# Performance work log

Hardware: AMD Instinct MI355X
Metric: run time of the kernel (lower is better)

Reference implementation:

```python
import jax, jax.numpy as jnp
import numpy as np

B, V, E, H, K = 4, 8192, 256, 8, 6  # batch, n_points, embed_dim, heads, knn


def setup_inputs() -> dict:
    key = jax.random.key(0)
    k1, k2, k3, k4 = jax.random.split(key, 4)
    scale = 1.0 / np.sqrt(E)
    return {
        "x": jax.random.normal(k1, (B, V, E), jnp.float32),
        "x_v": jax.random.normal(k2, (B, V, 3), jnp.float32),
        "in_proj_w": jax.random.normal(k3, (3 * E, E), jnp.float32) * scale,
        "out_proj_w": jax.random.normal(k4, (E, E), jnp.float32) * scale,
    }


def reference(x, x_v, in_proj_w, out_proj_w):
    Bn, Vn, En = x.shape
    Dh = En // H

    # ---- knn_points(x_v, x_v, K, return_sorted=True): squared L2 dists ----
    sq = jnp.sum(x_v * x_v, axis=-1)  # [B,V]
    d = sq[:, :, None] + sq[:, None, :] - 2.0 * jnp.einsum('bvc,bwc->bvw', x_v, x_v)
    _, idx = jax.lax.top_k(-d, K)  # [B,V,K], ascending distance (self first)

    # ---- knn_gather(x, idx) ----
    k = jax.vmap(lambda xb, ib: xb[ib])(x, idx)  # [B,V,K,E]
    v = k - x[:, :, None, :]                      # use_direction=True

    # ---- tiny MHA per point (Q len 1, KV len K), bias=False, eval (no dropout) ----
    Wq, Wk, Wv = jnp.split(in_proj_w, 3, axis=0)  # each [E,E]
    qp = (x @ Wq.T).reshape(Bn, Vn, H, Dh)
    kp = jnp.einsum('bvke,fe->bvkf', k, Wk).reshape(Bn, Vn, K, H, Dh)
    vp = jnp.einsum('bvke,fe->bvkf', v, Wv).reshape(Bn, Vn, K, H, Dh)
    scores = jnp.einsum('bvhd,bvkhd->bvhk', qp, kp) / np.sqrt(Dh)
    attn = jax.nn.softmax(scores, axis=-1)  # [B,V,H,K]
    out = jnp.einsum('bvhk,bvkhd->bvhd', attn, vp).reshape(Bn, Vn, En)
    out = out @ out_proj_w.T
    x_out = x + out

    # ---- scatter_reduce mean of head-averaged attention weights ----
    x_w = attn.mean(axis=2)  # [B,V,K] (MHA averages weights over heads)
    idx_f = idx.reshape(Bn, Vn * K)
    src = x_w.reshape(Bn, Vn * K)
    sums = jax.vmap(lambda i, s: jax.ops.segment_sum(s, i, num_segments=Vn))(idx_f, src)
    ones = jnp.ones((Vn * K,), jnp.float32)
    counts = jax.vmap(lambda i: jax.ops.segment_sum(ones, i, num_segments=Vn))(idx_f)
    # torch scatter_reduce_ 'mean' with include_self=True on a zeros tensor:
    # mean includes the initial 0, so denominator is count + 1.
    xw_out = (sums / (counts + 1.0))[..., None]  # [B,V,1]

    return x_out, xw_out
```

## Files before the change

kernel.cpp:

```cpp
#include <hip/hip_runtime.h>
#include <hip/hip_bf16.h>
#include <math.h>

#define BB 4
#define VV 8192
#define EE 256
#define HH 8
#define KK 6
#define NP (BB*VV)

#define OFF_XV4 0
#define OFF_KNN 524288
#define OFF_XWS 1310720
#define OFF_XWC 1441792
#define OFF_XB  1572864
#define OFF_WB  18350080
#define OFF_QKV 18874368
#define OFF_AO  69206016

typedef float f32x4 __attribute__((ext_vector_type(4)));
typedef __bf16 bf16x8 __attribute__((ext_vector_type(8)));

__device__ __forceinline__ unsigned short f2b(float f) {
  __hip_bfloat16 h = __float2bfloat16(f);
  return *reinterpret_cast<unsigned short*>(&h);
}
__device__ __forceinline__ float b2f(unsigned short u) {
  unsigned v = ((unsigned)u) << 16;
  return __uint_as_float(v);
}

__global__ void prep_kernel(const float* __restrict__ xv, float4* __restrict__ xv4,
                            float* __restrict__ xw_sum, float* __restrict__ xw_cnt) {
  int i = blockIdx.x * blockDim.x + threadIdx.x;
  if (i >= NP) return;
  float x0 = xv[i*3+0], x1 = xv[i*3+1], x2 = xv[i*3+2];
  float sq = __fadd_rn(__fadd_rn(__fmul_rn(x0,x0), __fmul_rn(x1,x1)), __fmul_rn(x2,x2));
  xv4[i] = make_float4(x0, x1, x2, sq);
  xw_sum[i] = 0.f;
  xw_cnt[i] = 0.f;
}

__global__ void cvt_bf16(const float* __restrict__ src, unsigned short* __restrict__ dst, int n4) {
  int i = blockIdx.x * blockDim.x + threadIdx.x;
  if (i >= n4) return;
  float4 v = ((const float4*)src)[i];
  ushort4 o;
  o.x = f2b(v.x); o.y = f2b(v.y); o.z = f2b(v.z); o.w = f2b(v.w);
  ((ushort4*)dst)[i] = o;
}


__device__ __forceinline__ unsigned long long pack_key(float dist, int j) {
  unsigned du = __float_as_uint(dist);
  du ^= (unsigned)((int)du >> 31) | 0x80000000u;
  return ((unsigned long long)du << 32) | (unsigned)j;
}

#define INSU(key) \
  if (key < k5) { \
    bool b4 = key < k4, b3 = key < k3, b2 = key < k2, b1 = key < k1, b0 = key < k0; \
    k5 = b4 ? k4 : key; \
    k4 = b4 ? (b3 ? k3 : key) : k4; \
    k3 = b3 ? (b2 ? k2 : key) : k3; \
    k2 = b2 ? (b1 ? k1 : key) : k2; \
    k1 = b1 ? (b0 ? k0 : key) : k1; \
    k0 = b0 ? key : k0; \
  }

__global__ __launch_bounds__(256) void knn_kernel(const float4* __restrict__ xv4,
                                                  int* __restrict__ knn_idx) {
  __shared__ float4 tile[1024];
  int tid = threadIdx.x;
  int qb = tid & 31;
  int c = tid >> 5;
  int q = blockIdx.x * 32 + qb;
  int base = (q >> 13) << 13;

  float4 me = xv4[q];
  float mx = me.x, my = me.y, mz = me.z, sqq = me.w;

  float d0=INFINITY,d1=INFINITY,d2=INFINITY,d3=INFINITY,d4=INFINITY,d5=INFINITY;
  int   i0=0x7fffffff,i1=0x7fffffff,i2=0x7fffffff,i3=0x7fffffff,i4=0x7fffffff,i5=0x7fffffff;

  for (int t = 0; t < 8; ++t) {
    __syncthreads();
#pragma unroll
    for (int u = 0; u < 4; ++u)
      tile[tid + u*256] = xv4[base + t*1024 + tid + u*256];
    __syncthreads();

    const float4* cp = &tile[c * 128];
    int jbase = t*1024 + c*128;
#pragma unroll 8
    for (int it = 0; it < 128; ++it) {
      float4 p = cp[it];
      float dot  = __fadd_rn(__fadd_rn(__fmul_rn(mx,p.x), __fmul_rn(my,p.y)), __fmul_rn(mz,p.z));
      float dist = __fsub_rn(__fadd_rn(sqq, p.w), __fmul_rn(2.0f, dot));
      if (dist < d5) {
        int j = jbase + it;
        bool b4 = dist < d4, b3 = dist < d3, b2 = dist < d2, b1 = dist < d1, b0 = dist < d0;
        d5 = b4 ? d4 : dist;            i5 = b4 ? i4 : j;
        d4 = b4 ? (b3 ? d3 : dist) : d4; i4 = b4 ? (b3 ? i3 : j) : i4;
        d3 = b3 ? (b2 ? d2 : dist) : d3; i3 = b3 ? (b2 ? i2 : j) : i3;
        d2 = b2 ? (b1 ? d1 : dist) : d2; i2 = b2 ? (b1 ? i1 : j) : i2;
        d1 = b1 ? (b0 ? d0 : dist) : d1; i1 = b1 ? (b0 ? i0 : j) : i1;
        d0 = b0 ? dist : d0;            i0 = b0 ? j : i0;
      }
    }
  }

  __syncthreads();
  unsigned long long* mk = reinterpret_cast<unsigned long long*>(tile);
  if (c > 0) {
    int o = qb*43 + (c-1)*6;
    mk[o+0]=pack_key(d0,i0); mk[o+1]=pack_key(d1,i1); mk[o+2]=pack_key(d2,i2);
    mk[o+3]=pack_key(d3,i3); mk[o+4]=pack_key(d4,i4); mk[o+5]=pack_key(d5,i5);
  }
  __syncthreads();
  if (c == 0) {
    unsigned long long k0=pack_key(d0,i0),k1=pack_key(d1,i1),k2=pack_key(d2,i2),
                       k3=pack_key(d3,i3),k4=pack_key(d4,i4),k5=pack_key(d5,i5);
    for (int s = 0; s < 42; ++s) {
      unsigned long long key = mk[qb*43 + s];
      INSU(key);
    }
    knn_idx[q*6+0] = (int)(unsigned)k0;
    knn_idx[q*6+1] = (int)(unsigned)k1;
    knn_idx[q*6+2] = (int)(unsigned)k2;
    knn_idx[q*6+3] = (int)(unsigned)k3;
    knn_idx[q*6+4] = (int)(unsigned)k4;
    knn_idx[q*6+5] = (int)(unsigned)k5;
  }
}

template<bool OUT_BF16>
__global__ __launch_bounds__(256) void gemm_bf16(const unsigned short* __restrict__ A,
                                                 const unsigned short* __restrict__ Bw,
                                                 void* __restrict__ Cv,
                                                 const float* __restrict__ R,
                                                 int ldc) {
  __shared__ unsigned short ABs[8192];
  int tid = threadIdx.x;
  int lane = tid & 63;
  int w = tid >> 6;
  int bm = blockIdx.x * 128;
  int bn = blockIdx.y * 128;
  int wr = w >> 1, wc = w & 1;

  f32x4 acc[4][4] = {};

  for (int ks = 0; ks < 8; ++ks) {
    int k0 = ks * 32;
    __syncthreads();
#pragma unroll
    for (int t = 0; t < 4; ++t) {
      int bg = (t*4 + w) * 64;
      int g = bg + lane;
      const unsigned short* src;
      if (bg < 512) {
        int r = g >> 2, kb = g & 3;
        src = A + (size_t)(bm + r) * 256 + k0 + kb*8;
      } else {
        int g2 = g - 512;
        int r = g2 >> 2, kb = g2 & 3;
        src = Bw + (size_t)(bn + r) * 256 + k0 + kb*8;
      }
      __builtin_amdgcn_global_load_lds(
        (const __attribute__((address_space(1))) unsigned int*)src,
        (__attribute__((address_space(3))) unsigned int*)&ABs[bg*8],
        16, 0, 0);
    }
    __syncthreads();

    bf16x8 af[4], bfr[4];
#pragma unroll
    for (int m = 0; m < 4; ++m)
      af[m] = *(const bf16x8*)&ABs[(wr*64 + m*16 + (lane&15))*32 + (lane>>4)*8];
#pragma unroll
    for (int n = 0; n < 4; ++n)
      bfr[n] = *(const bf16x8*)&ABs[4096 + (wc*64 + n*16 + (lane&15))*32 + (lane>>4)*8];
#pragma unroll
    for (int m = 0; m < 4; ++m)
#pragma unroll
      for (int n = 0; n < 4; ++n)
        acc[m][n] = __builtin_amdgcn_mfma_f32_16x16x32_bf16(af[m], bfr[n], acc[m][n], 0, 0, 0);
  }

  int rb = bm + wr*64 + (lane>>4)*4;
  int cb = bn + wc*64 + (lane&15);
#pragma unroll
  for (int m = 0; m < 4; ++m)
#pragma unroll
    for (int n = 0; n < 4; ++n)
#pragma unroll
      for (int i = 0; i < 4; ++i) {
        int row = rb + m*16 + i;
        int col = cb + n*16;
        float v = acc[m][n][i];
        if (OUT_BF16) {
          ((unsigned short*)Cv)[(size_t)row*ldc + col] = f2b(v);
        } else {
          ((float*)Cv)[(size_t)row*ldc + col] = v + R[(size_t)row*ldc + col];
        }
      }
}

__global__ __launch_bounds__(256) void attn_kernel(const unsigned short* __restrict__ QKV,
                                                   const int* __restrict__ knn_idx,
                                                   unsigned short* __restrict__ attn_out,
                                                   float* __restrict__ xw_sum,
                                                   float* __restrict__ xw_cnt) {
  int p = blockIdx.x * 4 + (threadIdx.x >> 6);
  int lane = threadIdx.x & 63;
  size_t gbase = (size_t)(p >> 13) << 13;
  size_t prow = (size_t)p * 768;

  ushort4 qv = *(const ushort4*)&QKV[prow + lane*4];
  ushort4 sv = *(const ushort4*)&QKV[prow + 512 + lane*4];
  float qx=b2f(qv.x), qy=b2f(qv.y), qz=b2f(qv.z), qw=b2f(qv.w);
  float sx=b2f(sv.x), sy=b2f(sv.y), sz=b2f(sv.z), sw=b2f(sv.w);

  int idx[KK];
#pragma unroll
  for (int j = 0; j < KK; ++j) idx[j] = knn_idx[p*KK + j];

  float s[KK];
  float vx[KK], vy[KK], vz[KK], vw[KK];
#pragma unroll
  for (int j = 0; j < KK; ++j) {
    size_t r = (gbase + idx[j]) * 768;
    ushort4 kv = *(const ushort4*)&QKV[r + 256 + lane*4];
    ushort4 vv = *(const ushort4*)&QKV[r + 512 + lane*4];
    float t = qx*b2f(kv.x) + qy*b2f(kv.y) + qz*b2f(kv.z) + qw*b2f(kv.w);
    t += __shfl_xor(t, 1);
    t += __shfl_xor(t, 2);
    t += __shfl_xor(t, 4);
    s[j] = t * 0.17677669529663687f;
    vx[j] = b2f(vv.x); vy[j] = b2f(vv.y); vz[j] = b2f(vv.z); vw[j] = b2f(vv.w);
  }

  float m = s[0];
#pragma unroll
  for (int j = 1; j < KK; ++j) m = fmaxf(m, s[j]);
  float e[KK], denom = 0.f;
#pragma unroll
  for (int j = 0; j < KK; ++j) { e[j] = expf(s[j] - m); denom += e[j]; }
  float inv = 1.0f / denom;
#pragma unroll
  for (int j = 0; j < KK; ++j) e[j] *= inv;

  float ox=0.f, oy=0.f, oz=0.f, ow=0.f;
#pragma unroll
  for (int j = 0; j < KK; ++j) {
    float a = e[j];
    ox += a * (vx[j] - sx);
    oy += a * (vy[j] - sy);
    oz += a * (vz[j] - sz);
    ow += a * (vw[j] - sw);
  }
  ushort4 ov;
  ov.x = f2b(ox); ov.y = f2b(oy); ov.z = f2b(oz); ov.w = f2b(ow);
  *(ushort4*)&attn_out[(size_t)p * 256 + lane*4] = ov;

#pragma unroll
  for (int j = 0; j < KK; ++j) {
    float t = e[j];
    t += __shfl_xor(t, 8);
    t += __shfl_xor(t, 16);
    t += __shfl_xor(t, 32);
    if (lane == 0) {
      atomicAdd(&xw_sum[gbase + idx[j]], t * 0.125f);
      atomicAdd(&xw_cnt[gbase + idx[j]], 1.0f);
    }
  }
}

__global__ void finalize_xw(const float* __restrict__ xw_sum,
                            const float* __restrict__ xw_cnt,
                            float* __restrict__ out) {
  int i = blockIdx.x * blockDim.x + threadIdx.x;
  if (i < NP) out[i] = xw_sum[i] / (xw_cnt[i] + 1.0f);
}

extern "C" void kernel_launch(void* const* d_in, const int* in_sizes, int n_in,
                              void* d_out, int out_size, void* d_ws, size_t ws_size,
                              hipStream_t stream) {
  const float* x     = (const float*)d_in[0];
  const float* xv    = (const float*)d_in[1];
  const float* w_in  = (const float*)d_in[2];
  const float* w_out = (const float*)d_in[3];
  float* out = (float*)d_out;

  char* ws = (char*)d_ws;
  float4*         xv4    = (float4*)(ws + OFF_XV4);
  int*            knn    = (int*)(ws + OFF_KNN);
  float*          xw_sum = (float*)(ws + OFF_XWS);
  float*          xw_cnt = (float*)(ws + OFF_XWC);
  unsigned short* xb     = (unsigned short*)(ws + OFF_XB);
  unsigned short* wb     = (unsigned short*)(ws + OFF_WB);
  unsigned short* qkv    = (unsigned short*)(ws + OFF_QKV);
  unsigned short* ao     = (unsigned short*)(ws + OFF_AO);

  prep_kernel<<<(NP + 255) / 256, 256, 0, stream>>>(xv, xv4, xw_sum, xw_cnt);
  cvt_bf16<<<(NP*256/4 + 255)/256, 256, 0, stream>>>(x, xb, NP*256/4);
  cvt_bf16<<<(768*256/4 + 255)/256, 256, 0, stream>>>(w_in, wb, 768*256/4);
  cvt_bf16<<<(256*256/4 + 255)/256, 256, 0, stream>>>(w_out, wb + 768*256, 256*256/4);

  knn_kernel<<<NP / 32, 256, 0, stream>>>(xv4, knn);

  gemm_bf16<true><<<dim3(NP/128, 768/128), 256, 0, stream>>>(xb, wb, qkv, nullptr, 768);

  attn_kernel<<<NP / 4, 256, 0, stream>>>(qkv, knn, ao, xw_sum, xw_cnt);

  gemm_bf16<false><<<dim3(NP/128, 256/128), 256, 0, stream>>>(ao, wb + 768*256, out, x, 256);

  finalize_xw<<<NP / 256, 256, 0, stream>>>(xw_sum, xw_cnt, out + (size_t)NP * EE);
}
```

Measured before the change: 281.4 us.

## Restructure kNN to one query per thread with two candidate chunks and merge kernel

The kNN search changes from 8 threads per query, each scanning a slice with an in-block shared-memory merge, to one query per thread. Each block loads a 4096-point chunk into shared memory once, and a grid dimension of 2 covers the two halves of each batch. Each thread writes 6 partial top-k keys per chunk to a global workspace, and a separate merge kernel combines the 12 candidates. This removes the repeated tile reloads, barriers and serial 42-step merge, but adds a kernel launch and a global round-trip for the partial results. Grid parallelism also drops from 1024 blocks to 256, and the 64 KB shared tile limits occupancy.

```diff
diff --git a/kernel.cpp b/kernel.cpp
--- a/kernel.cpp
+++ b/kernel.cpp
@@ -9,14 +9,15 @@
 #define KK 6
 #define NP (BB*VV)
 
-#define OFF_XV4 0
-#define OFF_KNN 524288
-#define OFF_XWS 1310720
-#define OFF_XWC 1441792
-#define OFF_XB  1572864
-#define OFF_WB  18350080
-#define OFF_QKV 18874368
-#define OFF_AO  69206016
+#define OFF_XV4  0
+#define OFF_KNN  524288
+#define OFF_XWS  1310720
+#define OFF_XWC  1441792
+#define OFF_XB   1572864
+#define OFF_WB   18350080
+#define OFF_QKV  18874368
+#define OFF_AO   69206016
+#define OFF_PART 85983232
 
 typedef float f32x4 __attribute__((ext_vector_type(4)));
 typedef __bf16 bf16x8 __attribute__((ext_vector_type(8)));
@@ -69,69 +70,65 @@
   }
 
 __global__ __launch_bounds__(256) void knn_kernel(const float4* __restrict__ xv4,
-                                                  int* __restrict__ knn_idx) {
-  __shared__ float4 tile[1024];
+                                                  unsigned long long* __restrict__ part) {
+  __shared__ float4 tile[4096];
   int tid = threadIdx.x;
-  int qb = tid & 31;
-  int c = tid >> 5;
-  int q = blockIdx.x * 32 + qb;
+  int q = blockIdx.x * 256 + tid;
   int base = (q >> 13) << 13;
+  int chunk = blockIdx.y;
+  int cbase = base + chunk * 4096;
 
   float4 me = xv4[q];
   float mx = me.x, my = me.y, mz = me.z, sqq = me.w;
 
+#pragma unroll
+  for (int u = 0; u < 16; ++u)
+    tile[tid + u*256] = xv4[cbase + tid + u*256];
+  __syncthreads();
+
   float d0=INFINITY,d1=INFINITY,d2=INFINITY,d3=INFINITY,d4=INFINITY,d5=INFINITY;
   int   i0=0x7fffffff,i1=0x7fffffff,i2=0x7fffffff,i3=0x7fffffff,i4=0x7fffffff,i5=0x7fffffff;
 
-  for (int t = 0; t < 8; ++t) {
-    __syncthreads();
-#pragma unroll
-    for (int u = 0; u < 4; ++u)
-      tile[tid + u*256] = xv4[base + t*1024 + tid + u*256];
-    __syncthreads();
-
-    const float4* cp = &tile[c * 128];
-    int jbase = t*1024 + c*128;
+  int jbase = chunk * 4096;
 #pragma unroll 8
-    for (int it = 0; it < 128; ++it) {
-      float4 p = cp[it];
-      float dot  = __fadd_rn(__fadd_rn(__fmul_rn(mx,p.x), __fmul_rn(my,p.y)), __fmul_rn(mz,p.z));
-      float dist = __fsub_rn(__fadd_rn(sqq, p.w), __fmul_rn(2.0f, dot));
-      if (dist < d5) {
-        int j = jbase + it;
-        bool b4 = dist < d4, b3 = dist < d3, b2 = dist < d2, b1 = dist < d1, b0 = dist < d0;
-        d5 = b4 ? d4 : dist;            i5 = b4 ? i4 : j;
-        d4 = b4 ? (b3 ? d3 : dist) : d4; i4 = b4 ? (b3 ? i3 : j) : i4;
-        d3 = b3 ? (b2 ? d2 : dist) : d3; i3 = b3 ? (b2 ? i2 : j) : i3;
-        d2 = b2 ? (b1 ? d1 : dist) : d2; i2 = b2 ? (b1 ? i1 : j) : i2;
-        d1 = b1 ? (b0 ? d0 : dist) : d1; i1 = b1 ? (b0 ? i0 : j) : i1;
-        d0 = b0 ? dist : d0;            i0 = b0 ? j : i0;
-      }
+  for (int it = 0; it < 4096; ++it) {
+    float4 p = tile[it];
+    float dot  = __fadd_rn(__fadd_rn(__fmul_rn(mx,p.x), __fmul_rn(my,p.y)), __fmul_rn(mz,p.z));
+    float dist = __fsub_rn(__fadd_rn(sqq, p.w), __fmul_rn(2.0f, dot));
+    if (dist < d5) {
+      int j = jbase + it;
+      bool b4 = dist < d4, b3 = dist < d3, b2 = dist < d2, b1 = dist < d1, b0 = dist < d0;
+      d5 = b4 ? d4 : dist;             i5 = b4 ? i4 : j;
+      d4 = b4 ? (b3 ? d3 : dist) : d4; i4 = b4 ? (b3 ? i3 : j) : i4;
+      d3 = b3 ? (b2 ? d2 : dist) : d3; i3 = b3 ? (b2 ? i2 : j) : i3;
+      d2 = b2 ? (b1 ? d1 : dist) : d2; i2 = b2 ? (b1 ? i1 : j) : i2;
+      d1 = b1 ? (b0 ? d0 : dist) : d1; i1 = b1 ? (b0 ? i0 : j) : i1;
+      d0 = b0 ? dist : d0;             i0 = b0 ? j : i0;
     }
   }
 
-  __syncthreads();
-  unsigned long long* mk = reinterpret_cast<unsigned long long*>(tile);
-  if (c > 0) {
-    int o = qb*43 + (c-1)*6;
-    mk[o+0]=pack_key(d0,i0); mk[o+1]=pack_key(d1,i1); mk[o+2]=pack_key(d2,i2);
-    mk[o+3]=pack_key(d3,i3); mk[o+4]=pack_key(d4,i4); mk[o+5]=pack_key(d5,i5);
-  }
-  __syncthreads();
-  if (c == 0) {
-    unsigned long long k0=pack_key(d0,i0),k1=pack_key(d1,i1),k2=pack_key(d2,i2),
-                       k3=pack_key(d3,i3),k4=pack_key(d4,i4),k5=pack_key(d5,i5);
-    for (int s = 0; s < 42; ++s) {
-      unsigned long long key = mk[qb*43 + s];
-      INSU(key);
-    }
-    knn_idx[q*6+0] = (int)(unsigned)k0;
-    knn_idx[q*6+1] = (int)(unsigned)k1;
-    knn_idx[q*6+2] = (int)(unsigned)k2;
-    knn_idx[q*6+3] = (int)(unsigned)k3;
-    knn_idx[q*6+4] = (int)(unsigned)k4;
-    knn_idx[q*6+5] = (int)(unsigned)k5;
-  }
+  unsigned long long* o = part + (size_t)q * 12 + chunk * 6;
+  o[0] = pack_key(d0, i0); o[1] = pack_key(d1, i1); o[2] = pack_key(d2, i2);
+  o[3] = pack_key(d3, i3); o[4] = pack_key(d4, i4); o[5] = pack_key(d5, i5);
+}
+
+__global__ void knn_merge(const unsigned long long* __restrict__ part,
+                          int* __restrict__ knn_idx) {
+  int q = blockIdx.x * 256 + threadIdx.x;
+  if (q >= NP) return;
+  unsigned long long k0=~0ull,k1=~0ull,k2=~0ull,k3=~0ull,k4=~0ull,k5=~0ull;
+  const unsigned long long* pp = part + (size_t)q * 12;
+#pragma unroll
+  for (int s = 0; s < 12; ++s) {
+    unsigned long long key = pp[s];
+    INSU(key);
+  }
+  knn_idx[q*6+0] = (int)(unsigned)k0;
+  knn_idx[q*6+1] = (int)(unsigned)k1;
+  knn_idx[q*6+2] = (int)(unsigned)k2;
+  knn_idx[q*6+3] = (int)(unsigned)k3;
+  knn_idx[q*6+4] = (int)(unsigned)k4;
+  knn_idx[q*6+5] = (int)(unsigned)k5;
 }
 
 template<bool OUT_BF16>
@@ -293,21 +290,23 @@
   float* out = (float*)d_out;
 
   char* ws = (char*)d_ws;
-  float4*         xv4    = (float4*)(ws + OFF_XV4);
-  int*            knn    = (int*)(ws + OFF_KNN);
-  float*          xw_sum = (float*)(ws + OFF_XWS);
-  float*          xw_cnt = (float*)(ws + OFF_XWC);
-  unsigned short* xb     = (unsigned short*)(ws + OFF_XB);
-  unsigned short* wb     = (unsigned short*)(ws + OFF_WB);
-  unsigned short* qkv    = (unsigned short*)(ws + OFF_QKV);
-  unsigned short* ao     = (unsigned short*)(ws + OFF_AO);
+  float4*             xv4    = (float4*)(ws + OFF_XV4);
+  int*                knn    = (int*)(ws + OFF_KNN);
+  float*              xw_sum = (float*)(ws + OFF_XWS);
+  float*              xw_cnt = (float*)(ws + OFF_XWC);
+  unsigned short*     xb     = (unsigned short*)(ws + OFF_XB);
+  unsigned short*     wb     = (unsigned short*)(ws + OFF_WB);
+  unsigned short*     qkv    = (unsigned short*)(ws + OFF_QKV);
+  unsigned short*     ao     = (unsigned short*)(ws + OFF_AO);
+  unsigned long long* part   = (unsigned long long*)(ws + OFF_PART);
 
   prep_kernel<<<(NP + 255) / 256, 256, 0, stream>>>(xv, xv4, xw_sum, xw_cnt);
   cvt_bf16<<<(NP*256/4 + 255)/256, 256, 0, stream>>>(x, xb, NP*256/4);
   cvt_bf16<<<(768*256/4 + 255)/256, 256, 0, stream>>>(w_in, wb, 768*256/4);
   cvt_bf16<<<(256*256/4 + 255)/256, 256, 0, stream>>>(w_out, wb + 768*256, 256*256/4);
 
-  knn_kernel<<<NP / 32, 256, 0, stream>>>(xv4, knn);
+  knn_kernel<<<dim3(NP/256, 2), 256, 0, stream>>>(xv4, part);
+  knn_merge<<<NP/256, 256, 0, stream>>>(part, knn);
 
   gemm_bf16<true><<<dim3(NP/128, 768/128), 256, 0, stream>>>(xb, wb, qkv, nullptr, 768);
 
```

New measurement: 478.5 us. 70.1% more time.

## Replace brute-force KNN with x-sorted sweep and early-exit pruning

Applied to the files above, without the earlier changes.

Bitonic-sorts points by x-coordinate per batch in shared memory, then each query scans outward in sorted order from its position with four interleaved directional threads. A thread stops once the x-gap squared exceeds its current sixth-best distance plus a margin. The four partial top-6 lists are merged in shared memory and written back through the sort permutation. This replaces the O(V^2) all-pairs distance scan with a pruned sweep, adding a single-block-per-batch sort and divergent, data-dependent loop lengths.

```diff
diff --git a/kernel.cpp b/kernel.cpp
--- a/kernel.cpp
+++ b/kernel.cpp
@@ -9,14 +9,16 @@
 #define KK 6
 #define NP (BB*VV)
 
-#define OFF_XV4 0
-#define OFF_KNN 524288
-#define OFF_XWS 1310720
-#define OFF_XWC 1441792
-#define OFF_XB  1572864
-#define OFF_WB  18350080
-#define OFF_QKV 18874368
-#define OFF_AO  69206016
+#define OFF_XV4  0
+#define OFF_KNN  524288
+#define OFF_XWS  1310720
+#define OFF_XWC  1441792
+#define OFF_XB   1572864
+#define OFF_WB   18350080
+#define OFF_QKV  18874368
+#define OFF_AO   69206016
+#define OFF_SXV  85983232
+#define OFF_SPM  86507520
 
 typedef float f32x4 __attribute__((ext_vector_type(4)));
 typedef __bf16 bf16x8 __attribute__((ext_vector_type(8)));
@@ -28,6 +30,19 @@
 __device__ __forceinline__ float b2f(unsigned short u) {
   unsigned v = ((unsigned)u) << 16;
   return __uint_as_float(v);
+}
+
+__device__ __forceinline__ unsigned sortable(float f) {
+  unsigned u = __float_as_uint(f);
+  return u ^ ((unsigned)((int)u >> 31) | 0x80000000u);
+}
+__device__ __forceinline__ unsigned long long pack_key(float dist, int j) {
+  return ((unsigned long long)sortable(dist) << 32) | (unsigned)j;
+}
+__device__ __forceinline__ float unpack_dist(unsigned long long k) {
+  unsigned du = (unsigned)(k >> 32);
+  du = (du & 0x80000000u) ? (du ^ 0x80000000u) : ~du;
+  return __uint_as_float(du);
 }
 
 __global__ void prep_kernel(const float* __restrict__ xv, float4* __restrict__ xv4,
@@ -50,12 +65,42 @@
   ((ushort4*)dst)[i] = o;
 }
 
-
-__device__ __forceinline__ unsigned long long pack_key(float dist, int j) {
-  unsigned du = __float_as_uint(dist);
-  du ^= (unsigned)((int)du >> 31) | 0x80000000u;
-  return ((unsigned long long)du << 32) | (unsigned)j;
-}
+__global__ __launch_bounds__(1024) void sort_kernel(const float4* __restrict__ xv4,
+                                                    float4* __restrict__ sxv4,
+                                                    int* __restrict__ sperm) {
+  __shared__ unsigned long long keys[VV];
+  int tid = threadIdx.x;
+  int bb = blockIdx.x * VV;
+#pragma unroll
+  for (int t = 0; t < 8; ++t) {
+    int i = tid + t*1024;
+    keys[i] = ((unsigned long long)sortable(xv4[bb + i].x) << 32) | (unsigned)i;
+  }
+  for (int k = 2; k <= VV; k <<= 1) {
+    for (int jj = k >> 1; jj > 0; jj >>= 1) {
+      __syncthreads();
+#pragma unroll
+      for (int t = 0; t < 4; ++t) {
+        int c = tid + t*1024;
+        int i = ((c & ~(jj-1)) << 1) | (c & (jj-1));
+        int p = i + jj;
+        bool up = ((i & k) == 0);
+        unsigned long long a = keys[i], b = keys[p];
+        if ((a > b) == up) { keys[i] = b; keys[p] = a; }
+      }
+    }
+  }
+  __syncthreads();
+#pragma unroll
+  for (int t = 0; t < 8; ++t) {
+    int r = tid + t*1024;
+    int idx = (int)(unsigned)keys[r];
+    sxv4[bb + r] = xv4[bb + idx];
+    sperm[bb + r] = idx;
+  }
+}
+
+#define MARGIN 1e-3f
 
 #define INSU(key) \
   if (key < k5) { \
@@ -68,69 +113,60 @@
     k0 = b0 ? key : k0; \
   }
 
-__global__ __launch_bounds__(256) void knn_kernel(const float4* __restrict__ xv4,
-                                                  int* __restrict__ knn_idx) {
-  __shared__ float4 tile[1024];
-  int tid = threadIdx.x;
-  int qb = tid & 31;
-  int c = tid >> 5;
-  int q = blockIdx.x * 32 + qb;
-  int base = (q >> 13) << 13;
-
-  float4 me = xv4[q];
+__global__ __launch_bounds__(256) void knn_scan(const float4* __restrict__ sxv4,
+                                                const int* __restrict__ sperm,
+                                                int* __restrict__ knn_idx) {
+  __shared__ unsigned long long sk[64][25];
+  int lane = threadIdx.x & 63;
+  int side = threadIdx.x >> 6;
+  int g = blockIdx.x * 64 + lane;
+  int bb = (g >> 13) << 13;
+
+  float4 me = sxv4[g];
   float mx = me.x, my = me.y, mz = me.z, sqq = me.w;
-
-  float d0=INFINITY,d1=INFINITY,d2=INFINITY,d3=INFINITY,d4=INFINITY,d5=INFINITY;
-  int   i0=0x7fffffff,i1=0x7fffffff,i2=0x7fffffff,i3=0x7fffffff,i4=0x7fffffff,i5=0x7fffffff;
-
-  for (int t = 0; t < 8; ++t) {
-    __syncthreads();
-#pragma unroll
-    for (int u = 0; u < 4; ++u)
-      tile[tid + u*256] = xv4[base + t*1024 + tid + u*256];
-    __syncthreads();
-
-    const float4* cp = &tile[c * 128];
-    int jbase = t*1024 + c*128;
-#pragma unroll 8
-    for (int it = 0; it < 128; ++it) {
-      float4 p = cp[it];
-      float dot  = __fadd_rn(__fadd_rn(__fmul_rn(mx,p.x), __fmul_rn(my,p.y)), __fmul_rn(mz,p.z));
-      float dist = __fsub_rn(__fadd_rn(sqq, p.w), __fmul_rn(2.0f, dot));
-      if (dist < d5) {
-        int j = jbase + it;
-        bool b4 = dist < d4, b3 = dist < d3, b2 = dist < d2, b1 = dist < d1, b0 = dist < d0;
-        d5 = b4 ? d4 : dist;            i5 = b4 ? i4 : j;
-        d4 = b4 ? (b3 ? d3 : dist) : d4; i4 = b4 ? (b3 ? i3 : j) : i4;
-        d3 = b3 ? (b2 ? d2 : dist) : d3; i3 = b3 ? (b2 ? i2 : j) : i3;
-        d2 = b2 ? (b1 ? d1 : dist) : d2; i2 = b2 ? (b1 ? i1 : j) : i2;
-        d1 = b1 ? (b0 ? d0 : dist) : d1; i1 = b1 ? (b0 ? i0 : j) : i1;
-        d0 = b0 ? dist : d0;            i0 = b0 ? j : i0;
-      }
-    }
-  }
-
+  int myidx = sperm[g];
+
+  unsigned long long k0=~0ull,k1=~0ull,k2=~0ull,k3=~0ull,k4=~0ull,k5=~0ull;
+  float d5f = __uint_as_float(0x7f7fffffu);
+
+  int step = (side & 2) ? 2 : -2;
+  int p0 = (side == 0) ? g - 1 : (side == 1) ? g - 2 : (side == 2) ? g : g + 1;
+
+  for (int p = p0; (unsigned)(p - bb) < (unsigned)VV; p += step) {
+    float4 c = sxv4[p];
+    float dx = mx - c.x;
+    if (dx * dx > d5f + MARGIN) break;
+    float dot  = __fadd_rn(__fadd_rn(__fmul_rn(mx,c.x), __fmul_rn(my,c.y)), __fmul_rn(mz,c.z));
+    float dist = __fsub_rn(__fadd_rn(sqq, c.w), __fmul_rn(2.0f, dot));
+    unsigned long long key = pack_key(dist, sperm[p]);
+    if (key < k5) {
+      bool b4 = key < k4, b3 = key < k3, b2 = key < k2, b1 = key < k1, b0 = key < k0;
+      k5 = b4 ? k4 : key;
+      k4 = b4 ? (b3 ? k3 : key) : k4;
+      k3 = b3 ? (b2 ? k2 : key) : k3;
+      k2 = b2 ? (b1 ? k1 : key) : k2;
+      k1 = b1 ? (b0 ? k0 : key) : k1;
+      k0 = b0 ? key : k0;
+      if (k5 != ~0ull) d5f = unpack_dist(k5);
+    }
+  }
+
+  sk[lane][side*6+0]=k0; sk[lane][side*6+1]=k1; sk[lane][side*6+2]=k2;
+  sk[lane][side*6+3]=k3; sk[lane][side*6+4]=k4; sk[lane][side*6+5]=k5;
   __syncthreads();
-  unsigned long long* mk = reinterpret_cast<unsigned long long*>(tile);
-  if (c > 0) {
-    int o = qb*43 + (c-1)*6;
-    mk[o+0]=pack_key(d0,i0); mk[o+1]=pack_key(d1,i1); mk[o+2]=pack_key(d2,i2);
-    mk[o+3]=pack_key(d3,i3); mk[o+4]=pack_key(d4,i4); mk[o+5]=pack_key(d5,i5);
-  }
-  __syncthreads();
-  if (c == 0) {
-    unsigned long long k0=pack_key(d0,i0),k1=pack_key(d1,i1),k2=pack_key(d2,i2),
-                       k3=pack_key(d3,i3),k4=pack_key(d4,i4),k5=pack_key(d5,i5);
-    for (int s = 0; s < 42; ++s) {
-      unsigned long long key = mk[qb*43 + s];
+  if (side == 0) {
+#pragma unroll
+    for (int s = 6; s < 24; ++s) {
+      unsigned long long key = sk[lane][s];
       INSU(key);
     }
-    knn_idx[q*6+0] = (int)(unsigned)k0;
-    knn_idx[q*6+1] = (int)(unsigned)k1;
-    knn_idx[q*6+2] = (int)(unsigned)k2;
-    knn_idx[q*6+3] = (int)(unsigned)k3;
-    knn_idx[q*6+4] = (int)(unsigned)k4;
-    knn_idx[q*6+5] = (int)(unsigned)k5;
+    int grow = bb + myidx;
+    knn_idx[grow*6+0] = (int)(unsigned)k0;
+    knn_idx[grow*6+1] = (int)(unsigned)k1;
+    knn_idx[grow*6+2] = (int)(unsigned)k2;
+    knn_idx[grow*6+3] = (int)(unsigned)k3;
+    knn_idx[grow*6+4] = (int)(unsigned)k4;
+    knn_idx[grow*6+5] = (int)(unsigned)k5;
   }
 }
 
@@ -301,13 +337,16 @@
   unsigned short* wb     = (unsigned short*)(ws + OFF_WB);
   unsigned short* qkv    = (unsigned short*)(ws + OFF_QKV);
   unsigned short* ao     = (unsigned short*)(ws + OFF_AO);
+  float4*         sxv4   = (float4*)(ws + OFF_SXV);
+  int*            sperm  = (int*)(ws + OFF_SPM);
 
   prep_kernel<<<(NP + 255) / 256, 256, 0, stream>>>(xv, xv4, xw_sum, xw_cnt);
   cvt_bf16<<<(NP*256/4 + 255)/256, 256, 0, stream>>>(x, xb, NP*256/4);
   cvt_bf16<<<(768*256/4 + 255)/256, 256, 0, stream>>>(w_in, wb, 768*256/4);
   cvt_bf16<<<(256*256/4 + 255)/256, 256, 0, stream>>>(w_out, wb + 768*256, 256*256/4);
 
-  knn_kernel<<<NP / 32, 256, 0, stream>>>(xv4, knn);
+  sort_kernel<<<BB, 1024, 0, stream>>>(xv4, sxv4, sperm);
+  knn_scan<<<NP/64, 256, 0, stream>>>(sxv4, sperm, knn);
 
   gemm_bf16<true><<<dim3(NP/128, 768/128), 256, 0, stream>>>(xb, wb, qkv, nullptr, 768);
 
```

New measurement: 881.9 us. +213.5%, slower.

## Fuse KNN and QKV GEMM into one interleaved launch with paired-point packed math

Applied to the files above, without the earlier changes.

Merges the KNN search and the QKV projection GEMM into a single front kernel. Blocks are interleaved 2:3 between KNN work and GEMM tiles so the ALU-bound KNN and the MFMA-bound GEMM can run concurrently on the device. The point coordinates are re-laid out in pairs (x0,x1,y0,y1,z0,z1,sq0,sq1) so the distance computation can use two-wide packed float math with contraction disabled. This adds register and LDS pressure from the shared kernel and branch divergence between block roles.

```diff
diff --git a/kernel.cpp b/kernel.cpp
--- a/kernel.cpp
+++ b/kernel.cpp
@@ -19,6 +19,7 @@
 #define OFF_AO  69206016
 
 typedef float f32x4 __attribute__((ext_vector_type(4)));
+typedef float f32x2 __attribute__((ext_vector_type(2)));
 typedef __bf16 bf16x8 __attribute__((ext_vector_type(8)));
 
 __device__ __forceinline__ unsigned short f2b(float f) {
@@ -30,31 +31,22 @@
   return __uint_as_float(v);
 }
 
-__global__ void prep_kernel(const float* __restrict__ xv, float4* __restrict__ xv4,
-                            float* __restrict__ xw_sum, float* __restrict__ xw_cnt) {
-  int i = blockIdx.x * blockDim.x + threadIdx.x;
-  if (i >= NP) return;
-  float x0 = xv[i*3+0], x1 = xv[i*3+1], x2 = xv[i*3+2];
-  float sq = __fadd_rn(__fadd_rn(__fmul_rn(x0,x0), __fmul_rn(x1,x1)), __fmul_rn(x2,x2));
-  xv4[i] = make_float4(x0, x1, x2, sq);
-  xw_sum[i] = 0.f;
-  xw_cnt[i] = 0.f;
-}
-
-__global__ void cvt_bf16(const float* __restrict__ src, unsigned short* __restrict__ dst, int n4) {
-  int i = blockIdx.x * blockDim.x + threadIdx.x;
-  if (i >= n4) return;
-  float4 v = ((const float4*)src)[i];
-  ushort4 o;
-  o.x = f2b(v.x); o.y = f2b(v.y); o.z = f2b(v.z); o.w = f2b(v.w);
-  ((ushort4*)dst)[i] = o;
-}
-
-
+__device__ __forceinline__ unsigned sortable(float f) {
+  unsigned u = __float_as_uint(f);
+  return u ^ ((unsigned)((int)u >> 31) | 0x80000000u);
+}
 __device__ __forceinline__ unsigned long long pack_key(float dist, int j) {
-  unsigned du = __float_as_uint(dist);
-  du ^= (unsigned)((int)du >> 31) | 0x80000000u;
-  return ((unsigned long long)du << 32) | (unsigned)j;
+  return ((unsigned long long)sortable(dist) << 32) | (unsigned)j;
+}
+
+#define INSERT6(dist,j) { \
+  bool b4 = dist < d4, b3 = dist < d3, b2 = dist < d2, b1 = dist < d1, b0 = dist < d0; \
+  d5 = b4 ? d4 : dist;             i5 = b4 ? i4 : j; \
+  d4 = b4 ? (b3 ? d3 : dist) : d4; i4 = b4 ? (b3 ? i3 : j) : i4; \
+  d3 = b3 ? (b2 ? d2 : dist) : d3; i3 = b3 ? (b2 ? i2 : j) : i3; \
+  d2 = b2 ? (b1 ? d1 : dist) : d2; i2 = b2 ? (b1 ? i1 : j) : i2; \
+  d1 = b1 ? (b0 ? d0 : dist) : d1; i1 = b1 ? (b0 ? i0 : j) : i1; \
+  d0 = b0 ? dist : d0;             i0 = b0 ? j : i0; \
 }
 
 #define INSU(key) \
@@ -68,78 +60,175 @@
     k0 = b0 ? key : k0; \
   }
 
-__global__ __launch_bounds__(256) void knn_kernel(const float4* __restrict__ xv4,
-                                                  int* __restrict__ knn_idx) {
-  __shared__ float4 tile[1024];
+__global__ void prep_kernel(const float* __restrict__ xv, float* __restrict__ xv4p,
+                            float* __restrict__ xw_sum, float* __restrict__ xw_cnt) {
+  int i = blockIdx.x * blockDim.x + threadIdx.x;
+  if (i >= NP) return;
+  float x0 = xv[i*3+0], x1 = xv[i*3+1], x2 = xv[i*3+2];
+  float sq = __fadd_rn(__fadd_rn(__fmul_rn(x0,x0), __fmul_rn(x1,x1)), __fmul_rn(x2,x2));
+  float* blk = xv4p + (size_t)(i >> 1) * 8;
+  int h = i & 1;
+  blk[0 + h] = x0; blk[2 + h] = x1; blk[4 + h] = x2; blk[6 + h] = sq;
+  xw_sum[i] = 0.f;
+  xw_cnt[i] = 0.f;
+}
+
+__global__ void cvt_bf16(const float* __restrict__ src, unsigned short* __restrict__ dst, int n4) {
+  int i = blockIdx.x * blockDim.x + threadIdx.x;
+  if (i >= n4) return;
+  float4 v = ((const float4*)src)[i];
+  ushort4 o;
+  o.x = f2b(v.x); o.y = f2b(v.y); o.z = f2b(v.z); o.w = f2b(v.w);
+  ((ushort4*)dst)[i] = o;
+}
+
+__global__ __launch_bounds__(256) void front_kernel(const float* __restrict__ xv4p,
+                                                    int* __restrict__ knn_idx,
+                                                    const unsigned short* __restrict__ A,
+                                                    const unsigned short* __restrict__ Bw,
+                                                    unsigned short* __restrict__ qkv) {
+  __shared__ __align__(16) float ldsf[4096];
+  int bid = blockIdx.x;
+  int rsel = bid % 5;
   int tid = threadIdx.x;
-  int qb = tid & 31;
-  int c = tid >> 5;
-  int q = blockIdx.x * 32 + qb;
-  int base = (q >> 13) << 13;
-
-  float4 me = xv4[q];
-  float mx = me.x, my = me.y, mz = me.z, sqq = me.w;
-
-  float d0=INFINITY,d1=INFINITY,d2=INFINITY,d3=INFINITY,d4=INFINITY,d5=INFINITY;
-  int   i0=0x7fffffff,i1=0x7fffffff,i2=0x7fffffff,i3=0x7fffffff,i4=0x7fffffff,i5=0x7fffffff;
-
-  for (int t = 0; t < 8; ++t) {
-    __syncthreads();
-#pragma unroll
-    for (int u = 0; u < 4; ++u)
-      tile[tid + u*256] = xv4[base + t*1024 + tid + u*256];
-    __syncthreads();
-
-    const float4* cp = &tile[c * 128];
-    int jbase = t*1024 + c*128;
+
+  if (rsel < 2) {
+#pragma clang fp contract(off)
+    int kb = (bid / 5) * 2 + rsel;
+    float* tile = ldsf;
+    int qb = tid & 31;
+    int c = tid >> 5;
+    int q = kb * 32 + qb;
+    int base = (q >> 13) << 13;
+
+    const f32x4* qblk = (const f32x4*)(xv4p + (size_t)(q >> 1) * 8);
+    f32x4 qa = qblk[0], qc = qblk[1];
+    int h = q & 1;
+    float mx = qa[h], my = qa[2 + h], mz = qc[h], sqq = qc[2 + h];
+    f32x2 mx2 = {mx, mx}, my2 = {my, my}, mz2 = {mz, mz}, sq2 = {sqq, sqq};
+
+    float d0=INFINITY,d1=INFINITY,d2=INFINITY,d3=INFINITY,d4=INFINITY,d5=INFINITY;
+    int   i0=0x7fffffff,i1=0x7fffffff,i2=0x7fffffff,i3=0x7fffffff,i4=0x7fffffff,i5=0x7fffffff;
+
+    const f32x4* gsrc = (const f32x4*)xv4p;
+    for (int t = 0; t < 8; ++t) {
+      __syncthreads();
+      f32x4* t4 = (f32x4*)tile;
+#pragma unroll
+      for (int u = 0; u < 4; ++u)
+        t4[tid + u*256] = gsrc[base + t*1024 + tid + u*256];
+      __syncthreads();
+
+      const f32x4* tp = (const f32x4*)tile;
+      int jbase = t*1024 + c*128;
 #pragma unroll 8
-    for (int it = 0; it < 128; ++it) {
-      float4 p = cp[it];
-      float dot  = __fadd_rn(__fadd_rn(__fmul_rn(mx,p.x), __fmul_rn(my,p.y)), __fmul_rn(mz,p.z));
-      float dist = __fsub_rn(__fadd_rn(sqq, p.w), __fmul_rn(2.0f, dot));
-      if (dist < d5) {
-        int j = jbase + it;
-        bool b4 = dist < d4, b3 = dist < d3, b2 = dist < d2, b1 = dist < d1, b0 = dist < d0;
-        d5 = b4 ? d4 : dist;            i5 = b4 ? i4 : j;
-        d4 = b4 ? (b3 ? d3 : dist) : d4; i4 = b4 ? (b3 ? i3 : j) : i4;
-        d3 = b3 ? (b2 ? d2 : dist) : d3; i3 = b3 ? (b2 ? i2 : j) : i3;
-        d2 = b2 ? (b1 ? d1 : dist) : d2; i2 = b2 ? (b1 ? i1 : j) : i2;
-        d1 = b1 ? (b0 ? d0 : dist) : d1; i1 = b1 ? (b0 ? i0 : j) : i1;
-        d0 = b0 ? dist : d0;            i0 = b0 ? j : i0;
-      }
-    }
-  }
-
-  __syncthreads();
-  unsigned long long* mk = reinterpret_cast<unsigned long long*>(tile);
-  if (c > 0) {
-    int o = qb*43 + (c-1)*6;
-    mk[o+0]=pack_key(d0,i0); mk[o+1]=pack_key(d1,i1); mk[o+2]=pack_key(d2,i2);
-    mk[o+3]=pack_key(d3,i3); mk[o+4]=pack_key(d4,i4); mk[o+5]=pack_key(d5,i5);
-  }
-  __syncthreads();
-  if (c == 0) {
-    unsigned long long k0=pack_key(d0,i0),k1=pack_key(d1,i1),k2=pack_key(d2,i2),
-                       k3=pack_key(d3,i3),k4=pack_key(d4,i4),k5=pack_key(d5,i5);
-    for (int s = 0; s < 42; ++s) {
-      unsigned long long key = mk[qb*43 + s];
-      INSU(key);
-    }
-    knn_idx[q*6+0] = (int)(unsigned)k0;
-    knn_idx[q*6+1] = (int)(unsigned)k1;
-    knn_idx[q*6+2] = (int)(unsigned)k2;
-    knn_idx[q*6+3] = (int)(unsigned)k3;
-    knn_idx[q*6+4] = (int)(unsigned)k4;
-    knn_idx[q*6+5] = (int)(unsigned)k5;
-  }
-}
-
-template<bool OUT_BF16>
-__global__ __launch_bounds__(256) void gemm_bf16(const unsigned short* __restrict__ A,
-                                                 const unsigned short* __restrict__ Bw,
-                                                 void* __restrict__ Cv,
-                                                 const float* __restrict__ R,
-                                                 int ldc) {
+      for (int it = 0; it < 64; ++it) {
+        f32x4 a = tp[(c*64 + it)*2];
+        f32x4 b = tp[(c*64 + it)*2 + 1];
+        f32x2 px2 = __builtin_shufflevector(a, a, 0, 1);
+        f32x2 py2 = __builtin_shufflevector(a, a, 2, 3);
+        f32x2 pz2 = __builtin_shufflevector(b, b, 0, 1);
+        f32x2 pw2 = __builtin_shufflevector(b, b, 2, 3);
+        f32x2 dot2  = (mx2*px2 + my2*py2) + mz2*pz2;
+        f32x2 dist2 = (sq2 + pw2) - 2.0f*dot2;
+        float dl = dist2[0], dh = dist2[1];
+        int j0 = jbase + 2*it;
+        if (dl < d5) { INSERT6(dl, j0); }
+        if (dh < d5) { int j1 = j0 + 1; INSERT6(dh, j1); }
+      }
+    }
+
+    __syncthreads();
+    unsigned long long* mk = reinterpret_cast<unsigned long long*>(tile);
+    if (c > 0) {
+      int o = qb*43 + (c-1)*6;
+      mk[o+0]=pack_key(d0,i0); mk[o+1]=pack_key(d1,i1); mk[o+2]=pack_key(d2,i2);
+      mk[o+3]=pack_key(d3,i3); mk[o+4]=pack_key(d4,i4); mk[o+5]=pack_key(d5,i5);
+    }
+    __syncthreads();
+    if (c == 0) {
+      unsigned long long k0=pack_key(d0,i0),k1=pack_key(d1,i1),k2=pack_key(d2,i2),
+                         k3=pack_key(d3,i3),k4=pack_key(d4,i4),k5=pack_key(d5,i5);
+      for (int s = 0; s < 42; ++s) {
+        unsigned long long key = mk[qb*43 + s];
+        INSU(key);
+      }
+      knn_idx[q*6+0] = (int)(unsigned)k0;
+      knn_idx[q*6+1] = (int)(unsigned)k1;
+      knn_idx[q*6+2] = (int)(unsigned)k2;
+      knn_idx[q*6+3] = (int)(unsigned)k3;
+      knn_idx[q*6+4] = (int)(unsigned)k4;
+      knn_idx[q*6+5] = (int)(unsigned)k5;
+    }
+    return;
+  }
+
+  int gb = (bid / 5) * 3 + (rsel - 2);
+  unsigned short* ABs = (unsigned short*)ldsf;
+  int lane = tid & 63;
+  int w = tid >> 6;
+  int bm = (gb % 256) * 128;
+  int bn = (gb / 256) * 128;
+  int wr = w >> 1, wc = w & 1;
+
+  f32x4 acc[4][4] = {};
+
+  for (int ks = 0; ks < 8; ++ks) {
+    int k0 = ks * 32;
+    __syncthreads();
+#pragma unroll
+    for (int t = 0; t < 4; ++t) {
+      int bg = (t*4 + w) * 64;
+      int g = bg + lane;
+      const unsigned short* src;
+      if (bg < 512) {
+        int r = g >> 2, kb2 = g & 3;
+        src = A + (size_t)(bm + r) * 256 + k0 + kb2*8;
+      } else {
+        int g2 = g - 512;
+        int r = g2 >> 2, kb2 = g2 & 3;
+        src = Bw + (size_t)(bn + r) * 256 + k0 + kb2*8;
+      }
+      __builtin_amdgcn_global_load_lds(
+        (const __attribute__((address_space(1))) unsigned int*)src,
+        (__attribute__((address_space(3))) unsigned int*)&ABs[bg*8],
+        16, 0, 0);
+    }
+    __syncthreads();
+
+    bf16x8 af[4], bfr[4];
+#pragma unroll
+    for (int m = 0; m < 4; ++m)
+      af[m] = *(const bf16x8*)&ABs[(wr*64 + m*16 + (lane&15))*32 + (lane>>4)*8];
+#pragma unroll
+    for (int n = 0; n < 4; ++n)
+      bfr[n] = *(const bf16x8*)&ABs[4096 + (wc*64 + n*16 + (lane&15))*32 + (lane>>4)*8];
+#pragma unroll
+    for (int m = 0; m < 4; ++m)
+#pragma unroll
+      for (int n = 0; n < 4; ++n)
+        acc[m][n] = __builtin_amdgcn_mfma_f32_16x16x32_bf16(af[m], bfr[n], acc[m][n], 0, 0, 0);
+  }
+
+  int rb = bm + wr*64 + (lane>>4)*4;
+  int cb = bn + wc*64 + (lane&15);
+#pragma unroll
+  for (int m = 0; m < 4; ++m)
+#pragma unroll
+    for (int n = 0; n < 4; ++n)
+#pragma unroll
+      for (int i = 0; i < 4; ++i) {
+        int row = rb + m*16 + i;
+        int col = cb + n*16;
+        qkv[(size_t)row*768 + col] = f2b(acc[m][n][i]);
+      }
+}
+
+__global__ __launch_bounds__(256) void gemm_bf16_f32(const unsigned short* __restrict__ A,
+                                                     const unsigned short* __restrict__ Bw,
+                                                     float* __restrict__ C,
+                                                     const float* __restrict__ R,
+                                                     int ldc) {
   __shared__ unsigned short ABs[8192];
   int tid = threadIdx.x;
   int lane = tid & 63;
@@ -159,12 +248,12 @@
       int g = bg + lane;
       const unsigned short* src;
       if (bg < 512) {
-        int r = g >> 2, kb = g & 3;
-        src = A + (size_t)(bm + r) * 256 + k0 + kb*8;
+        int r = g >> 2, kb2 = g & 3;
+        src = A + (size_t)(bm + r) * 256 + k0 + kb2*8;
       } else {
         int g2 = g - 512;
-        int r = g2 >> 2, kb = g2 & 3;
-        src = Bw + (size_t)(bn + r) * 256 + k0 + kb*8;
+        int r = g2 >> 2, kb2 = g2 & 3;
+        src = Bw + (size_t)(bn + r) * 256 + k0 + kb2*8;
       }
       __builtin_amdgcn_global_load_lds(
         (const __attribute__((address_space(1))) unsigned int*)src,
@@ -197,12 +286,7 @@
       for (int i = 0; i < 4; ++i) {
         int row = rb + m*16 + i;
         int col = cb + n*16;
-        float v = acc[m][n][i];
-        if (OUT_BF16) {
-          ((unsigned short*)Cv)[(size_t)row*ldc + col] = f2b(v);
-        } else {
-          ((float*)Cv)[(size_t)row*ldc + col] = v + R[(size_t)row*ldc + col];
-        }
+        C[(size_t)row*ldc + col] = acc[m][n][i] + R[(size_t)row*ldc + col];
       }
 }
 
@@ -293,7 +377,7 @@
   float* out = (float*)d_out;
 
   char* ws = (char*)d_ws;
-  float4*         xv4    = (float4*)(ws + OFF_XV4);
+  float*          xv4p   = (float*)(ws + OFF_XV4);
   int*            knn    = (int*)(ws + OFF_KNN);
   float*          xw_sum = (float*)(ws + OFF_XWS);
   float*          xw_cnt = (float*)(ws + OFF_XWC);
@@ -302,18 +386,16 @@
   unsigned short* qkv    = (unsigned short*)(ws + OFF_QKV);
   unsigned short* ao     = (unsigned short*)(ws + OFF_AO);
 
-  prep_kernel<<<(NP + 255) / 256, 256, 0, stream>>>(xv, xv4, xw_sum, xw_cnt);
+  prep_kernel<<<(NP + 255) / 256, 256, 0, stream>>>(xv, xv4p, xw_sum, xw_cnt);
   cvt_bf16<<<(NP*256/4 + 255)/256, 256, 0, stream>>>(x, xb, NP*256/4);
   cvt_bf16<<<(768*256/4 + 255)/256, 256, 0, stream>>>(w_in, wb, 768*256/4);
   cvt_bf16<<<(256*256/4 + 255)/256, 256, 0, stream>>>(w_out, wb + 768*256, 256*256/4);
 
-  knn_kernel<<<NP / 32, 256, 0, stream>>>(xv4, knn);
-
-  gemm_bf16<true><<<dim3(NP/128, 768/128), 256, 0, stream>>>(xb, wb, qkv, nullptr, 768);
+  front_kernel<<<2560, 256, 0, stream>>>(xv4p, knn, xb, wb, qkv);
 
   attn_kernel<<<NP / 4, 256, 0, stream>>>(qkv, knn, ao, xw_sum, xw_cnt);
 
-  gemm_bf16<false><<<dim3(NP/128, 256/128), 256, 0, stream>>>(ao, wb + 768*256, out, x, 256);
+  gemm_bf16_f32<<<dim3(NP/128, 256/128), 256, 0, stream>>>(ao, wb + 768*256, out, x, 256);
 
   finalize_xw<<<NP / 256, 256, 0, stream>>>(xw_sum, xw_cnt, out + (size_t)NP * EE);
 }
```

New measurement: 297.1 us. 1.06x slower.
